# Optimization experiments

Hardware: AMD Instinct MI355X
Metric: run time of the kernel (lower is better)

## Reference

```python
import jax, jax.numpy as jnp
import numpy as np

HIDDEN = 4096
N_HEADS = 32
N_KV_HEADS = 8
HEAD_DIM = HIDDEN // N_HEADS  # 128
INTER = 11008
EPS = 1e-6
ROPE_THETA = 10000.0
B, S = 2, 2048


def setup_inputs() -> dict:
    key = jax.random.key(0)
    ks = jax.random.split(key, 8)
    sc = 0.02
    return {
        "hidden_states": jax.random.normal(ks[0], (B, S, HIDDEN), dtype=jnp.float32),
        "positions": jnp.arange(S, dtype=jnp.int32),
        "w_qkv": jax.random.normal(ks[1], (HIDDEN, (N_HEADS + 2 * N_KV_HEADS) * HEAD_DIM), dtype=jnp.float32) * sc,
        "w_o": jax.random.normal(ks[2], (N_HEADS * HEAD_DIM, HIDDEN), dtype=jnp.float32) * sc,
        "w_gate_up": jax.random.normal(ks[3], (HIDDEN, 2 * INTER), dtype=jnp.float32) * sc,
        "w_down": jax.random.normal(ks[4], (INTER, HIDDEN), dtype=jnp.float32) * sc,
        "ln1_w": jnp.ones((HIDDEN,), dtype=jnp.float32),
        "ln2_w": jnp.ones((HIDDEN,), dtype=jnp.float32),
    }


def _rms_norm(x, w):
    var = jnp.mean(jnp.square(x), axis=-1, keepdims=True)
    return x * jax.lax.rsqrt(var + EPS) * w


def _rope(x, positions):
    # x: [B, S, H, D]; NeoX-style rotary over full head_dim
    d = x.shape[-1]
    inv_freq = 1.0 / (ROPE_THETA ** (jnp.arange(0, d, 2, dtype=jnp.float32) / d))
    freqs = positions.astype(jnp.float32)[:, None] * inv_freq[None, :]  # [S, D/2]
    cos = jnp.cos(freqs)[None, :, None, :]
    sin = jnp.sin(freqs)[None, :, None, :]
    x1, x2 = jnp.split(x, 2, axis=-1)
    return jnp.concatenate([x1 * cos - x2 * sin, x2 * cos + x1 * sin], axis=-1)


def _decoder_layer(hidden_states, positions, w_qkv, w_o, w_gate_up, w_down, ln1_w, ln2_w):
    b, s, _ = hidden_states.shape
    scale = HEAD_DIM ** -0.5

    # --- attention block ---
    residual = hidden_states
    x = _rms_norm(hidden_states, ln1_w)
    qkv = x @ w_qkv
    q, k, v = jnp.split(qkv, [N_HEADS * HEAD_DIM, (N_HEADS + N_KV_HEADS) * HEAD_DIM], axis=-1)
    q = q.reshape(b, s, N_HEADS, HEAD_DIM)
    k = k.reshape(b, s, N_KV_HEADS, HEAD_DIM)
    v = v.reshape(b, s, N_KV_HEADS, HEAD_DIM)
    q = _rope(q, positions)
    k = _rope(k, positions)
    # GQA: expand kv heads
    g = N_HEADS // N_KV_HEADS
    k = jnp.repeat(k, g, axis=2)  # [B, S, H, D]
    v = jnp.repeat(v, g, axis=2)
    scores = jnp.einsum("bqhd,bkhd->bhqk", q, k) * scale
    causal = jnp.tril(jnp.ones((s, s), dtype=bool))
    scores = jnp.where(causal[None, None], scores, jnp.finfo(scores.dtype).min)
    probs = jax.nn.softmax(scores, axis=-1)
    attn = jnp.einsum("bhqk,bkhd->bqhd", probs, v).reshape(b, s, N_HEADS * HEAD_DIM)
    hidden_states = residual + attn @ w_o

    # --- MLP block (SwiGLU) ---
    residual = hidden_states
    x = _rms_norm(hidden_states, ln2_w)
    gate_up = x @ w_gate_up
    gate, up = jnp.split(gate_up, 2, axis=-1)
    hidden_states = residual + (jax.nn.silu(gate) * up) @ w_down
    return hidden_states


def reference(hidden_states, positions, w_qkv, w_o, w_gate_up, w_down, ln1_w, ln2_w):
    return _decoder_layer(hidden_states, positions, w_qkv, w_o, w_gate_up, w_down, ln1_w, ln2_w)
```

## Files before the change

### kernel.cpp

```cpp
#include <hip/hip_runtime.h>


typedef __attribute__((ext_vector_type(8))) short bf16x8;
typedef __attribute__((ext_vector_type(4))) float f32x4;

__device__ __forceinline__ ushort f2bf(float f) {
  unsigned u = __float_as_uint(f);
  return (ushort)((u + 0x7fffu + ((u >> 16) & 1u)) >> 16);
}
__device__ __forceinline__ float bf2f(ushort u) {
  union { unsigned u32; float f; } x; x.u32 = ((unsigned)u) << 16; return x.f;
}
__device__ __forceinline__ void gload16(const void* g, void* l) {
  __builtin_amdgcn_global_load_lds((__attribute__((address_space(1))) void*)g,
                                   (__attribute__((address_space(3))) void*)l,
                                   16, 0, 0);
}

#define BARRIER() asm volatile("s_barrier" ::: "memory")
#define WAIT_LGKM0() asm volatile("s_waitcnt lgkmcnt(0)" ::: "memory")
#define WAIT_VM8() asm volatile("s_waitcnt vmcnt(8)" ::: "memory")
#define WAIT_VM4() asm volatile("s_waitcnt vmcnt(4)" ::: "memory")
#define WAIT_VM0() asm volatile("s_waitcnt vmcnt(0)" ::: "memory")

__global__ __launch_bounds__(256) void rmsnorm_kernel(
    const float* __restrict__ x, const float* __restrict__ g,
    ushort* __restrict__ out) {
  const int row = blockIdx.x, t = threadIdx.x;
  const float4* xp = (const float4*)(x + (size_t)row * 4096);
  float4 v[4]; float ss = 0.f;
#pragma unroll
  for (int i = 0; i < 4; ++i) {
    v[i] = xp[t + i * 256];
    ss += v[i].x * v[i].x + v[i].y * v[i].y + v[i].z * v[i].z + v[i].w * v[i].w;
  }
#pragma unroll
  for (int m = 32; m; m >>= 1) ss += __shfl_xor(ss, m);
  __shared__ float red[4];
  if ((t & 63) == 0) red[t >> 6] = ss;
  __syncthreads();
  float inv = rsqrtf((red[0] + red[1] + red[2] + red[3]) * (1.f / 4096.f) + 1e-6f);
  const float4* gp = (const float4*)g;
  ushort* op = out + (size_t)row * 4096;
#pragma unroll
  for (int i = 0; i < 4; ++i) {
    float4 gv = gp[t + i * 256];
    ushort4 o;
    o.x = f2bf(v[i].x * inv * gv.x); o.y = f2bf(v[i].y * inv * gv.y);
    o.z = f2bf(v[i].z * inv * gv.z); o.w = f2bf(v[i].w * inv * gv.w);
    *(ushort4*)(op + (size_t)(t + i * 256) * 4) = o;
  }
}

__global__ __launch_bounds__(256) void transpose_cast_kernel(
    const float* __restrict__ in, ushort* __restrict__ out,
    int ld_in, int col_off, int R) {
  __shared__ ushort tile[64][68];
  const int t = threadIdx.x;
  const int r0 = blockIdx.x * 64, c0 = blockIdx.y * 64;
  const int rl = t >> 2, cl = (t & 3) * 16;
  const float* ip = in + (size_t)(r0 + rl) * ld_in + col_off + c0 + cl;
#pragma unroll
  for (int i = 0; i < 4; ++i) {
    float4 f = ((const float4*)ip)[i];
    tile[rl][cl + i * 4 + 0] = f2bf(f.x);
    tile[rl][cl + i * 4 + 1] = f2bf(f.y);
    tile[rl][cl + i * 4 + 2] = f2bf(f.z);
    tile[rl][cl + i * 4 + 3] = f2bf(f.w);
  }
  __syncthreads();
  union { ushort us[8]; uint4 v; } pk0, pk1;
#pragma unroll
  for (int j = 0; j < 8; ++j) pk0.us[j] = tile[cl + j][rl];
#pragma unroll
  for (int j = 0; j < 8; ++j) pk1.us[j] = tile[cl + 8 + j][rl];
  uint4* op = (uint4*)(out + (size_t)(c0 + rl) * R + r0 + cl);
  op[0] = pk0.v; op[1] = pk1.v;
}

template <typename OutT, bool RES>
__global__ __launch_bounds__(512, 2) void gemm256_kernel(
    const ushort* __restrict__ A, const ushort* __restrict__ Bt,
    OutT* __restrict__ C, const float* __restrict__ res,
    int M, int N, int K) {
  extern __shared__ ushort lds[];
  ushort* Al = lds;
  ushort* Bl = lds + 32768;
  const int t = threadIdx.x, l = t & 63, w = t >> 6;
  const int wr = w >> 2, wc = w & 3;
  const int lr = l & 15, lg = l >> 4;
  const int rhi = lr >> 3, rlo = lr & 7;
  const int srow = l >> 3, sg = (l & 7) ^ srow;

  const int nbx = N >> 8;
  const int nwg = nbx * (M >> 8);
  const int cpx = nwg >> 3;
  const int bid = (int)blockIdx.x;
  const int swz = (bid & 7) * cpx + (bid >> 3);
  const int n0 = (swz % nbx) << 8, m0 = (swz / nbx) << 8;

  const int lof0 = rhi * 512 + rlo * 64 + ((0 + lg) ^ rlo) * 8;
  const int lof1 = rhi * 512 + rlo * 64 + ((4 + lg) ^ rlo) * 8;

  const f32x4 fz = {0.f, 0.f, 0.f, 0.f};
  f32x4 acc[8][4];
#pragma unroll
  for (int i = 0; i < 8; ++i)
#pragma unroll
    for (int j = 0; j < 4; ++j) acc[i][j] = fz;
  bf16x8 a[8][2];
  bf16x8 bq[2][2];

  const ushort* Asrc = A + (size_t)(m0 + w * 8 + srow) * K + sg * 8;
  const ushort* Bsrc = Bt + (size_t)(n0 + w * 8 + srow) * K + sg * 8;
  const size_t rK64 = (size_t)64 * K, rK128 = (size_t)128 * K;
  ushort* Adst = Al + w * 512;
  ushort* Bdst = Bl + w * 512;

#define STAGE_A(buf, half, tile) do {                                   \
    const ushort* s_ = Asrc + (size_t)(half) * rK128 + ((tile) << 6);   \
    ushort* d_ = Adst + (buf) * 16384 + (half) * 8192;                  \
    gload16(s_, d_);                                                    \
    gload16(s_ + rK64, d_ + 4096);                                      \
  } while (0)
#define STAGE_B(buf, half, tile) do {                                   \
    const ushort* s_ = Bsrc + (size_t)(half) * rK128 + ((tile) << 6);   \
    ushort* d_ = Bdst + (buf) * 16384 + (half) * 8192;                  \
    gload16(s_, d_);                                                    \
    gload16(s_ + rK64, d_ + 4096);                                      \
  } while (0)
#define LDA4(AH, QM) do {                                                   \
    _Pragma("unroll") for (int mi_ = 0; mi_ < 4; ++mi_) {                   \
      a[(QM) * 4 + mi_][0] =                                                \
          *(const bf16x8*)((AH) + ((QM) * 4 + mi_) * 1024 + lof0);          \
      a[(QM) * 4 + mi_][1] =                                                \
          *(const bf16x8*)((AH) + ((QM) * 4 + mi_) * 1024 + lof1);          \
    } } while (0)
#define LDB2(BH, NQ) do {                                                   \
    _Pragma("unroll") for (int nj_ = 0; nj_ < 2; ++nj_) {                   \
      bq[nj_][0] = *(const bf16x8*)((BH) + ((NQ) * 2 + nj_) * 1024 + lof0); \
      bq[nj_][1] = *(const bf16x8*)((BH) + ((NQ) * 2 + nj_) * 1024 + lof1); \
    } } while (0)
#define MFMA16(QM, QN)                                                      \
    __builtin_amdgcn_s_setprio(1);                                          \
    _Pragma("unroll") for (int mi_ = 0; mi_ < 4; ++mi_)                     \
    _Pragma("unroll") for (int nj_ = 0; nj_ < 2; ++nj_) {                   \
      acc[(QM) * 4 + mi_][(QN) * 2 + nj_] =                                 \
          __builtin_amdgcn_mfma_f32_16x16x32_bf16(                          \
              a[(QM) * 4 + mi_][0], bq[nj_][0],                             \
              acc[(QM) * 4 + mi_][(QN) * 2 + nj_], 0, 0, 0);                \
      acc[(QM) * 4 + mi_][(QN) * 2 + nj_] =                                 \
          __builtin_amdgcn_mfma_f32_16x16x32_bf16(                          \
              a[(QM) * 4 + mi_][1], bq[nj_][1],                             \
              acc[(QM) * 4 + mi_][(QN) * 2 + nj_], 0, 0, 0);                \
    }                                                                       \
    __builtin_amdgcn_s_setprio(0);

  const ushort* A0h = Al + wr * 8192;
  const ushort* A1h = A0h + 16384;
  const ushort* B0h = Bl + (wc >> 1) * 8192 + (wc & 1) * 4096;
  const ushort* B1h = B0h + 16384;

  const int ntiles = K >> 6, nIter = K >> 7;
  STAGE_A(0, 0, 0); STAGE_A(0, 1, 0); STAGE_B(0, 0, 0); STAGE_B(0, 1, 0);
  STAGE_A(1, 0, 1); STAGE_A(1, 1, 1);
  WAIT_VM4(); BARRIER();

  for (int it = 0; it < nIter; ++it) {
    const int u = it * 2;
    LDA4(A0h, 0); LDB2(B0h, 0);
    STAGE_B(1, 0, u + 1);
    BARRIER(); WAIT_LGKM0(); MFMA16(0, 0); BARRIER();
    LDA4(A0h, 1);
    STAGE_B(1, 1, u + 1);
    BARRIER(); WAIT_LGKM0(); MFMA16(1, 0); BARRIER();
    LDB2(B0h, 1);
    if (u + 2 < ntiles) STAGE_A(0, 0, u + 2);
    BARRIER(); WAIT_LGKM0(); MFMA16(0, 1); BARRIER();
    if (u + 2 < ntiles) STAGE_A(0, 1, u + 2);
    BARRIER(); MFMA16(1, 1);
    if (u + 2 < ntiles) { WAIT_VM4(); } else { WAIT_VM0(); }
    BARRIER();
    LDA4(A1h, 0); LDB2(B1h, 0);
    if (u + 2 < ntiles) STAGE_B(0, 0, u + 2);
    BARRIER(); WAIT_LGKM0(); MFMA16(0, 0); BARRIER();
    LDA4(A1h, 1);
    if (u + 2 < ntiles) STAGE_B(0, 1, u + 2);
    BARRIER(); WAIT_LGKM0(); MFMA16(1, 0); BARRIER();
    LDB2(B1h, 1);
    if (u + 3 < ntiles) STAGE_A(1, 0, u + 3);
    BARRIER(); WAIT_LGKM0(); MFMA16(0, 1); BARRIER();
    if (u + 3 < ntiles) STAGE_A(1, 1, u + 3);
    BARRIER(); MFMA16(1, 1);
    WAIT_VM4(); BARRIER();
  }

#pragma unroll
  for (int mi = 0; mi < 8; ++mi)
#pragma unroll
    for (int ni = 0; ni < 4; ++ni)
#pragma unroll
      for (int r = 0; r < 4; ++r) {
        int row = m0 + wr * 128 + mi * 16 + lg * 4 + r;
        int col = n0 + wc * 64 + ni * 16 + lr;
        size_t idx = (size_t)row * N + col;
        float v = acc[mi][ni][r];
        if (RES) v += res[idx];
        if constexpr (sizeof(OutT) == 2) C[idx] = f2bf(v);
        else                             C[idx] = v;
      }
#undef STAGE_A
#undef STAGE_B
#undef LDA4
#undef LDB2
#undef MFMA16
}

__global__ void rope_table_kernel(const int* __restrict__ pos,
                                  float2* __restrict__ tab) {
  int idx = blockIdx.x * 256 + threadIdx.x;
  int s = idx >> 6, fi = idx & 63;
  float inv = (float)exp(-(double)(2 * fi) / 128.0 * 9.210340371976184);
  float a = (float)pos[s] * inv;
  tab[idx] = make_float2(cosf(a), sinf(a));
}

__global__ __launch_bounds__(256) void rope_scatter_kernel(
    const ushort* __restrict__ qkv, const float2* __restrict__ tab,
    ushort* __restrict__ Qr, ushort* __restrict__ Kr, ushort* __restrict__ Vt) {
  __shared__ ushort vt[64][132];
  const int t = threadIdx.x, tt = blockIdx.x, h = blockIdx.y;
  const int row = t >> 2, c = (t & 3) * 16;
  const int tok = tt * 64 + row;
  const int b = tok >> 11, s = tok & 2047;
  const ushort* ip = qkv + (size_t)tok * 6144 + h * 128;
  union U { uint4 v; ushort us[8]; };
  U a0, a1, b0, b1;
  a0.v = *(const uint4*)(ip + c);      a1.v = *(const uint4*)(ip + c + 8);
  b0.v = *(const uint4*)(ip + c + 64); b1.v = *(const uint4*)(ip + c + 72);
  if (h < 40) {
    U o0, o1, o2, o3;
#pragma unroll
    for (int j = 0; j < 8; ++j) {
      float2 cs = tab[s * 64 + c + j];
      float x1 = bf2f(a0.us[j]), x2 = bf2f(b0.us[j]);
      o0.us[j] = f2bf(x1 * cs.x - x2 * cs.y);
      o2.us[j] = f2bf(x2 * cs.x + x1 * cs.y);
    }
#pragma unroll
    for (int j = 0; j < 8; ++j) {
      float2 cs = tab[s * 64 + c + 8 + j];
      float x1 = bf2f(a1.us[j]), x2 = bf2f(b1.us[j]);
      o1.us[j] = f2bf(x1 * cs.x - x2 * cs.y);
      o3.us[j] = f2bf(x2 * cs.x + x1 * cs.y);
    }
    ushort* base;
    if (h < 32) base = Qr + ((size_t)((b * 32 + h) * 2048 + s)) * 128;
    else        base = Kr + ((size_t)((b * 8 + (h - 32)) * 2048 + s)) * 128;
    *(uint4*)(base + c)      = o0.v; *(uint4*)(base + c + 8)  = o1.v;
    *(uint4*)(base + c + 64) = o2.v; *(uint4*)(base + c + 72) = o3.v;
  } else {
    const int hv = h - 40;
#pragma unroll
    for (int j = 0; j < 8; ++j) {
      vt[row][c + j]      = a0.us[j]; vt[row][c + 8 + j]  = a1.us[j];
      vt[row][c + 64 + j] = b0.us[j]; vt[row][c + 72 + j] = b1.us[j];
    }
    __syncthreads();
    const int d = t >> 1, s0 = (t & 1) * 32, sb = (tt & 31) * 64;
    U w0, w1, w2, w3;
#pragma unroll
    for (int j = 0; j < 8; ++j) {
      w0.us[j] = vt[s0 + j][d];      w1.us[j] = vt[s0 + 8 + j][d];
      w2.us[j] = vt[s0 + 16 + j][d]; w3.us[j] = vt[s0 + 24 + j][d];
    }
    ushort* vb = Vt + ((size_t)((b * 8 + hv) * 128 + d)) * 2048 + sb + s0;
    *(uint4*)(vb) = w0.v;      *(uint4*)(vb + 8) = w1.v;
    *(uint4*)(vb + 16) = w2.v; *(uint4*)(vb + 24) = w3.v;
  }
}

__global__ __launch_bounds__(256) void attn_kernel(
    const ushort* __restrict__ Q, const ushort* __restrict__ K,
    const ushort* __restrict__ V, ushort* __restrict__ O) {
  extern __shared__ ushort sm[];
  ushort* Kl = sm;
  ushort* Vl = sm + 16384;
  ushort* Pl = sm + 32768;
  const int t = threadIdx.x, l = t & 63, w = t >> 6;
  const int lr = l & 15, lg = l >> 4;
  const int qt = blockIdx.x, h = blockIdx.y, b = blockIdx.z;
  const int hkv = h >> 2;
  const f32x4 fzero = {0.f, 0.f, 0.f, 0.f};

  const int rm = lr & 7;
  int ksw[4], vsw[2];
#pragma unroll
  for (int ks = 0; ks < 4; ++ks) ksw[ks] = ((ks * 4 + lg) ^ rm) * 8;
  vsw[0] = (lg ^ rm) * 8;
  vsw[1] = ((4 + lg) ^ rm) * 8;
  const int kcol = ((t & 15) ^ ((t >> 4) & 7)) * 8;
  const int vcol = ((t & 7) ^ ((t >> 3) & 7)) * 8;

  const ushort* qp =
      Q + ((size_t)((b * 32 + h) * 2048 + qt * 64 + w * 16 + lr)) * 128 + lg * 8;
  bf16x8 qf[4];
#pragma unroll
  for (int ks = 0; ks < 4; ++ks) qf[ks] = *(const bf16x8*)(qp + ks * 32);
  WAIT_VM0();

  const ushort* kg = K + ((size_t)(b * 8 + hkv)) * 2048 * 128;
  const ushort* vg = V + ((size_t)(b * 8 + hkv)) * 128 * 2048;

#define STAGE_KV(buf, s0_) do {                                              \
    _Pragma("unroll") for (int i_ = 0; i_ < 4; ++i_)                         \
      gload16(kg + (size_t)((s0_) + i_ * 16 + (t >> 4)) * 128 + kcol,        \
              (char*)Kl + (buf) * 16384 + i_ * 4096 + t * 16);               \
    _Pragma("unroll") for (int i_ = 0; i_ < 4; ++i_)                         \
      gload16(vg + (size_t)(i_ * 32 + (t >> 3)) * 2048 + (s0_) + vcol,       \
              (char*)Vl + (buf) * 16384 + i_ * 4096 + t * 16);               \
  } while (0)

  f32x4 accO[8];
#pragma unroll
  for (int i = 0; i < 8; ++i) accO[i] = fzero;
  float m_r[4] = {-1e30f, -1e30f, -1e30f, -1e30f};
  float l_r[4] = {0.f, 0.f, 0.f, 0.f};
  const float scale = 0.08838834764831845f;
  const int qrow = qt * 64 + w * 16 + lg * 4;

  STAGE_KV(0, 0);
  for (int j = 0; j <= qt; ++j) {
    if (j < qt) { STAGE_KV((j + 1) & 1, (j + 1) * 64); WAIT_VM8(); }
    else        { WAIT_VM0(); }
    BARRIER();
    const ushort* Kb = Kl + (j & 1) * 8192;
    const ushort* Vb = Vl + (j & 1) * 8192;

    f32x4 sc[4];
#pragma unroll
    for (int ni = 0; ni < 4; ++ni) sc[ni] = fzero;
    __builtin_amdgcn_s_setprio(1);
#pragma unroll
    for (int ni = 0; ni < 4; ++ni)
#pragma unroll
      for (int ks = 0; ks < 4; ++ks) {
        bf16x8 kf = *(const bf16x8*)(Kb + (ni * 16 + lr) * 128 + ksw[ks]);
        sc[ni] = __builtin_amdgcn_mfma_f32_16x16x32_bf16(qf[ks], kf, sc[ni], 0, 0, 0);
      }
    __builtin_amdgcn_s_setprio(0);
    if (j == qt) {
#pragma unroll
      for (int ni = 0; ni < 4; ++ni)
#pragma unroll
        for (int r = 0; r < 4; ++r) {
          float v = sc[ni][r] * scale;
          if (j * 64 + ni * 16 + lr > qrow + r) v = -1e30f;
          sc[ni][r] = v;
        }
    } else {
#pragma unroll
      for (int ni = 0; ni < 4; ++ni)
#pragma unroll
        for (int r = 0; r < 4; ++r) sc[ni][r] *= scale;
    }
    float mnew[4], fsc[4], lad[4];
#pragma unroll
    for (int r = 0; r < 4; ++r) {
      float mx = fmaxf(fmaxf(sc[0][r], sc[1][r]), fmaxf(sc[2][r], sc[3][r]));
#pragma unroll
      for (int m = 8; m; m >>= 1) mx = fmaxf(mx, __shfl_xor(mx, m));
      mnew[r] = fmaxf(m_r[r], mx);
      fsc[r] = __expf(m_r[r] - mnew[r]);
      lad[r] = 0.f;
    }
#pragma unroll
    for (int ni = 0; ni < 4; ++ni)
#pragma unroll
      for (int r = 0; r < 4; ++r) {
        float p = __expf(sc[ni][r] - mnew[r]);
        sc[ni][r] = p;
        lad[r] += p;
      }
#pragma unroll
    for (int r = 0; r < 4; ++r) {
#pragma unroll
      for (int m = 8; m; m >>= 1) lad[r] += __shfl_xor(lad[r], m);
      l_r[r] = l_r[r] * fsc[r] + lad[r];
      m_r[r] = mnew[r];
    }
#pragma unroll
    for (int i = 0; i < 8; ++i)
#pragma unroll
      for (int r = 0; r < 4; ++r) accO[i][r] *= fsc[r];
#pragma unroll
    for (int ni = 0; ni < 4; ++ni)
#pragma unroll
      for (int r = 0; r < 4; ++r) {
        int prow = w * 16 + lg * 4 + r;
        int slot = (ni * 2 + (lr >> 3)) ^ (prow & 7);
        Pl[prow * 64 + slot * 8 + rm] = f2bf(sc[ni][r]);
      }
    WAIT_LGKM0();
    __builtin_amdgcn_s_setprio(1);
#pragma unroll
    for (int ks = 0; ks < 2; ++ks) {
      bf16x8 pf = *(const bf16x8*)(Pl + (w * 16 + lr) * 64 + vsw[ks]);
#pragma unroll
      for (int nf = 0; nf < 8; ++nf) {
        bf16x8 vf = *(const bf16x8*)(Vb + (nf * 16 + lr) * 64 + vsw[ks]);
        accO[nf] = __builtin_amdgcn_mfma_f32_16x16x32_bf16(pf, vf, accO[nf], 0, 0, 0);
      }
    }
    __builtin_amdgcn_s_setprio(0);
    BARRIER();
  }
#undef STAGE_KV
#pragma unroll
  for (int nf = 0; nf < 8; ++nf)
#pragma unroll
    for (int r = 0; r < 4; ++r) {
      int q = qt * 64 + w * 16 + lg * 4 + r;
      int d = nf * 16 + lr;
      float v = accO[nf][r] / l_r[r];
      O[((size_t)(b * 2048 + q)) * 4096 + h * 128 + d] = f2bf(v);
    }
}

__global__ void swiglu_kernel(ushort* __restrict__ gate,
                              const ushort* __restrict__ up, int n8) {
  union U { uint4 v; ushort us[8]; };
  for (int i = blockIdx.x * blockDim.x + threadIdx.x; i < n8;
       i += gridDim.x * blockDim.x) {
    U gv, uv, ov;
    gv.v = ((const uint4*)gate)[i];
    uv.v = ((const uint4*)up)[i];
#pragma unroll
    for (int j = 0; j < 8; ++j) {
      float x = bf2f(gv.us[j]);
      float y = bf2f(uv.us[j]);
      ov.us[j] = f2bf(x / (1.f + __expf(-x)) * y);
    }
    ((uint4*)gate)[i] = ov.v;
  }
}

#define OFF_W    ((size_t)0)
#define OFF_H1   ((size_t)90177536)
#define OFF_XN   ((size_t)157286400)
#define OFF_QKV  ((size_t)190840832)
#define OFF_TAB  ((size_t)241172480)
#define OFF_QR   ((size_t)242221056)
#define OFF_KR   ((size_t)275775488)
#define OFF_VT   ((size_t)284164096)
#define OFF_ATTN ((size_t)292552704)
#define OFF_GATE OFF_QKV
#define OFF_UP   ((size_t)326107136)
#define WS_NEED  ((size_t)416284672)

extern "C" void kernel_launch(void* const* d_in, const int* in_sizes, int n_in,
                              void* d_out, int out_size, void* d_ws,
                              size_t ws_size, hipStream_t stream) {
  (void)in_sizes; (void)n_in; (void)out_size;
  if (ws_size < WS_NEED) return;
  const float* hs     = (const float*)d_in[0];
  const int*   pos    = (const int*)d_in[1];
  const float* w_qkv  = (const float*)d_in[2];
  const float* w_o    = (const float*)d_in[3];
  const float* w_gu   = (const float*)d_in[4];
  const float* w_down = (const float*)d_in[5];
  const float* ln1    = (const float*)d_in[6];
  const float* ln2    = (const float*)d_in[7];
  float* out = (float*)d_out;
  char* ws = (char*)d_ws;

  ushort* W    = (ushort*)(ws + OFF_W);
  float*  h1   = (float*)(ws + OFF_H1);
  ushort* xn   = (ushort*)(ws + OFF_XN);
  ushort* qkv  = (ushort*)(ws + OFF_QKV);
  float2* tab  = (float2*)(ws + OFF_TAB);
  ushort* Qr   = (ushort*)(ws + OFF_QR);
  ushort* Kr   = (ushort*)(ws + OFF_KR);
  ushort* Vt   = (ushort*)(ws + OFF_VT);
  ushort* attn = (ushort*)(ws + OFF_ATTN);
  ushort* gate = (ushort*)(ws + OFF_GATE);
  ushort* up   = (ushort*)(ws + OFF_UP);

  auto kb = gemm256_kernel<ushort, false>;
  auto kf = gemm256_kernel<float, true>;
  hipFuncSetAttribute((const void*)kb, hipFuncAttributeMaxDynamicSharedMemorySize, 131072);
  hipFuncSetAttribute((const void*)kf, hipFuncAttributeMaxDynamicSharedMemorySize, 131072);
  hipFuncSetAttribute((const void*)attn_kernel, hipFuncAttributeMaxDynamicSharedMemorySize, 73728);

  rmsnorm_kernel<<<4096, 256, 0, stream>>>(hs, ln1, xn);
  transpose_cast_kernel<<<dim3(64, 96), 256, 0, stream>>>(w_qkv, W, 6144, 0, 4096);
  gemm256_kernel<ushort, false><<<384, 512, 131072, stream>>>(
      xn, W, qkv, nullptr, 4096, 6144, 4096);
  rope_table_kernel<<<512, 256, 0, stream>>>(pos, tab);
  rope_scatter_kernel<<<dim3(64, 48), 256, 0, stream>>>(qkv, tab, Qr, Kr, Vt);
  attn_kernel<<<dim3(32, 32, 2), 256, 73728, stream>>>(Qr, Kr, Vt, attn);
  transpose_cast_kernel<<<dim3(64, 64), 256, 0, stream>>>(w_o, W, 4096, 0, 4096);
  gemm256_kernel<float, true><<<256, 512, 131072, stream>>>(
      attn, W, h1, hs, 4096, 4096, 4096);

  rmsnorm_kernel<<<4096, 256, 0, stream>>>(h1, ln2, xn);
  transpose_cast_kernel<<<dim3(64, 172), 256, 0, stream>>>(w_gu, W, 22016, 0, 4096);
  gemm256_kernel<ushort, false><<<688, 512, 131072, stream>>>(
      xn, W, gate, nullptr, 4096, 11008, 4096);
  transpose_cast_kernel<<<dim3(64, 172), 256, 0, stream>>>(w_gu, W, 22016, 11008, 4096);
  gemm256_kernel<ushort, false><<<688, 512, 131072, stream>>>(
      xn, W, up, nullptr, 4096, 11008, 4096);
  swiglu_kernel<<<2048, 256, 0, stream>>>(gate, up, (4096 * 11008) / 8);
  transpose_cast_kernel<<<dim3(172, 64), 256, 0, stream>>>(w_down, W, 4096, 0, 11008);
  gemm256_kernel<float, true><<<256, 512, 131072, stream>>>(
      gate, W, out, h1, 4096, 4096, 11008);
}
```

Measured before the change: 1.911 ms.

## Fuse SwiGLU into up GEMM epilogue and streamline attention softmax

The separate SwiGLU kernel is removed and its work moves into the up-projection GEMM epilogue, which reads the bf16 gate tensor and writes the activated product. Attention now folds the softmax scale and log2e into Q, uses exp2, skips the rescale when the running max grows by at most 8, and computes row sums with an extra MFMA against a ones vector instead of shuffle reductions. The transpose tile padding also changes from 68 to 65. The cost is slightly lower precision from pre-scaling Q in bf16 and from the lazy rescale, and the 65-wide tile may cause misaligned or bank-conflicting LDS accesses.

```diff
diff --git a/kernel.cpp b/kernel.cpp
--- a/kernel.cpp
+++ b/kernel.cpp
@@ -55,7 +55,7 @@
 __global__ __launch_bounds__(256) void transpose_cast_kernel(
     const float* __restrict__ in, ushort* __restrict__ out,
     int ld_in, int col_off, int R) {
-  __shared__ ushort tile[64][68];
+  __shared__ ushort tile[64][65];
   const int t = threadIdx.x;
   const int r0 = blockIdx.x * 64, c0 = blockIdx.y * 64;
   const int rl = t >> 2, cl = (t & 3) * 16;
@@ -78,10 +78,10 @@
   op[0] = pk0.v; op[1] = pk1.v;
 }
 
-template <typename OutT, bool RES>
+template <int EPI>
 __global__ __launch_bounds__(512, 2) void gemm256_kernel(
     const ushort* __restrict__ A, const ushort* __restrict__ Bt,
-    OutT* __restrict__ C, const float* __restrict__ res,
+    void* __restrict__ Cv, const void* __restrict__ aux,
     int M, int N, int K) {
   extern __shared__ ushort lds[];
   ushort* Al = lds;
@@ -205,9 +205,15 @@
         int col = n0 + wc * 64 + ni * 16 + lr;
         size_t idx = (size_t)row * N + col;
         float v = acc[mi][ni][r];
-        if (RES) v += res[idx];
-        if constexpr (sizeof(OutT) == 2) C[idx] = f2bf(v);
-        else                             C[idx] = v;
+        if constexpr (EPI == 0) {
+          ((ushort*)Cv)[idx] = f2bf(v);
+        } else if constexpr (EPI == 1) {
+          ((float*)Cv)[idx] = v + ((const float*)aux)[idx];
+        } else {
+          float g = bf2f(((const ushort*)aux)[idx]);
+          float s = g / (1.f + __expf(-g));
+          ((ushort*)Cv)[idx] = f2bf(s * v);
+        }
       }
 #undef STAGE_A
 #undef STAGE_B
@@ -302,11 +308,20 @@
   const int kcol = ((t & 15) ^ ((t >> 4) & 7)) * 8;
   const int vcol = ((t & 7) ^ ((t >> 3) & 7)) * 8;
 
+  const float qscale = 0.08838834764831845f * 1.4426950408889634f;
   const ushort* qp =
       Q + ((size_t)((b * 32 + h) * 2048 + qt * 64 + w * 16 + lr)) * 128 + lg * 8;
   bf16x8 qf[4];
 #pragma unroll
-  for (int ks = 0; ks < 4; ++ks) qf[ks] = *(const bf16x8*)(qp + ks * 32);
+  for (int ks = 0; ks < 4; ++ks) {
+    bf16x8 raw = *(const bf16x8*)(qp + ks * 32);
+#pragma unroll
+    for (int j = 0; j < 8; ++j)
+      qf[ks][j] = (short)f2bf(bf2f((ushort)raw[j]) * qscale);
+  }
+  bf16x8 ones;
+#pragma unroll
+  for (int j = 0; j < 8; ++j) ones[j] = (short)0x3F80;
   WAIT_VM0();
 
   const ushort* kg = K + ((size_t)(b * 8 + hkv)) * 2048 * 128;
@@ -326,7 +341,6 @@
   for (int i = 0; i < 8; ++i) accO[i] = fzero;
   float m_r[4] = {-1e30f, -1e30f, -1e30f, -1e30f};
   float l_r[4] = {0.f, 0.f, 0.f, 0.f};
-  const float scale = 0.08838834764831845f;
   const int qrow = qt * 64 + w * 16 + lg * 4;
 
   STAGE_KV(0, 0);
@@ -353,55 +367,40 @@
 #pragma unroll
       for (int ni = 0; ni < 4; ++ni)
 #pragma unroll
-        for (int r = 0; r < 4; ++r) {
-          float v = sc[ni][r] * scale;
-          if (j * 64 + ni * 16 + lr > qrow + r) v = -1e30f;
-          sc[ni][r] = v;
-        }
-    } else {
-#pragma unroll
-      for (int ni = 0; ni < 4; ++ni)
-#pragma unroll
-        for (int r = 0; r < 4; ++r) sc[ni][r] *= scale;
-    }
-    float mnew[4], fsc[4], lad[4];
+        for (int r = 0; r < 4; ++r)
+          if (j * 64 + ni * 16 + lr > qrow + r) sc[ni][r] = -1e30f;
+    }
+    float mx[4];
 #pragma unroll
     for (int r = 0; r < 4; ++r) {
-      float mx = fmaxf(fmaxf(sc[0][r], sc[1][r]), fmaxf(sc[2][r], sc[3][r]));
-#pragma unroll
-      for (int m = 8; m; m >>= 1) mx = fmaxf(mx, __shfl_xor(mx, m));
-      mnew[r] = fmaxf(m_r[r], mx);
-      fsc[r] = __expf(m_r[r] - mnew[r]);
-      lad[r] = 0.f;
-    }
-#pragma unroll
-    for (int ni = 0; ni < 4; ++ni)
+      float v = fmaxf(fmaxf(sc[0][r], sc[1][r]), fmaxf(sc[2][r], sc[3][r]));
+#pragma unroll
+      for (int m = 8; m; m >>= 1) v = fmaxf(v, __shfl_xor(v, m));
+      mx[r] = v;
+    }
+    bool ok = mx[0] <= m_r[0] + 8.f && mx[1] <= m_r[1] + 8.f &&
+              mx[2] <= m_r[2] + 8.f && mx[3] <= m_r[3] + 8.f;
+    if (!__all(ok)) {
 #pragma unroll
       for (int r = 0; r < 4; ++r) {
-        float p = __expf(sc[ni][r] - mnew[r]);
-        sc[ni][r] = p;
-        lad[r] += p;
+        float mnew = fmaxf(m_r[r], mx[r]);
+        float fsc = exp2f(m_r[r] - mnew);
+        l_r[r] *= fsc;
+        m_r[r] = mnew;
+#pragma unroll
+        for (int i = 0; i < 8; ++i) accO[i][r] *= fsc;
       }
-#pragma unroll
-    for (int r = 0; r < 4; ++r) {
-#pragma unroll
-      for (int m = 8; m; m >>= 1) lad[r] += __shfl_xor(lad[r], m);
-      l_r[r] = l_r[r] * fsc[r] + lad[r];
-      m_r[r] = mnew[r];
-    }
-#pragma unroll
-    for (int i = 0; i < 8; ++i)
-#pragma unroll
-      for (int r = 0; r < 4; ++r) accO[i][r] *= fsc[r];
+    }
 #pragma unroll
     for (int ni = 0; ni < 4; ++ni)
 #pragma unroll
       for (int r = 0; r < 4; ++r) {
         int prow = w * 16 + lg * 4 + r;
         int slot = (ni * 2 + (lr >> 3)) ^ (prow & 7);
-        Pl[prow * 64 + slot * 8 + rm] = f2bf(sc[ni][r]);
+        Pl[prow * 64 + slot * 8 + rm] = f2bf(exp2f(sc[ni][r] - m_r[r]));
       }
     WAIT_LGKM0();
+    f32x4 accL = fzero;
     __builtin_amdgcn_s_setprio(1);
 #pragma unroll
     for (int ks = 0; ks < 2; ++ks) {
@@ -411,8 +410,11 @@
         bf16x8 vf = *(const bf16x8*)(Vb + (nf * 16 + lr) * 64 + vsw[ks]);
         accO[nf] = __builtin_amdgcn_mfma_f32_16x16x32_bf16(pf, vf, accO[nf], 0, 0, 0);
       }
+      accL = __builtin_amdgcn_mfma_f32_16x16x32_bf16(pf, ones, accL, 0, 0, 0);
     }
     __builtin_amdgcn_s_setprio(0);
+#pragma unroll
+    for (int r = 0; r < 4; ++r) l_r[r] += accL[r];
     BARRIER();
   }
 #undef STAGE_KV
@@ -425,24 +427,6 @@
       float v = accO[nf][r] / l_r[r];
       O[((size_t)(b * 2048 + q)) * 4096 + h * 128 + d] = f2bf(v);
     }
-}
-
-__global__ void swiglu_kernel(ushort* __restrict__ gate,
-                              const ushort* __restrict__ up, int n8) {
-  union U { uint4 v; ushort us[8]; };
-  for (int i = blockIdx.x * blockDim.x + threadIdx.x; i < n8;
-       i += gridDim.x * blockDim.x) {
-    U gv, uv, ov;
-    gv.v = ((const uint4*)gate)[i];
-    uv.v = ((const uint4*)up)[i];
-#pragma unroll
-    for (int j = 0; j < 8; ++j) {
-      float x = bf2f(gv.us[j]);
-      float y = bf2f(uv.us[j]);
-      ov.us[j] = f2bf(x / (1.f + __expf(-x)) * y);
-    }
-    ((uint4*)gate)[i] = ov.v;
-  }
 }
 
 #define OFF_W    ((size_t)0)
@@ -484,34 +468,27 @@
   ushort* Vt   = (ushort*)(ws + OFF_VT);
   ushort* attn = (ushort*)(ws + OFF_ATTN);
   ushort* gate = (ushort*)(ws + OFF_GATE);
-  ushort* up   = (ushort*)(ws + OFF_UP);
-
-  auto kb = gemm256_kernel<ushort, false>;
-  auto kf = gemm256_kernel<float, true>;
-  hipFuncSetAttribute((const void*)kb, hipFuncAttributeMaxDynamicSharedMemorySize, 131072);
-  hipFuncSetAttribute((const void*)kf, hipFuncAttributeMaxDynamicSharedMemorySize, 131072);
+  ushort* act  = (ushort*)(ws + OFF_UP);
+
+  hipFuncSetAttribute((const void*)gemm256_kernel<0>, hipFuncAttributeMaxDynamicSharedMemorySize, 131072);
+  hipFuncSetAttribute((const void*)gemm256_kernel<1>, hipFuncAttributeMaxDynamicSharedMemorySize, 131072);
+  hipFuncSetAttribute((const void*)gemm256_kernel<2>, hipFuncAttributeMaxDynamicSharedMemorySize, 131072);
   hipFuncSetAttribute((const void*)attn_kernel, hipFuncAttributeMaxDynamicSharedMemorySize, 73728);
 
   rmsnorm_kernel<<<4096, 256, 0, stream>>>(hs, ln1, xn);
   transpose_cast_kernel<<<dim3(64, 96), 256, 0, stream>>>(w_qkv, W, 6144, 0, 4096);
-  gemm256_kernel<ushort, false><<<384, 512, 131072, stream>>>(
-      xn, W, qkv, nullptr, 4096, 6144, 4096);
+  gemm256_kernel<0><<<384, 512, 131072, stream>>>(xn, W, qkv, nullptr, 4096, 6144, 4096);
   rope_table_kernel<<<512, 256, 0, stream>>>(pos, tab);
   rope_scatter_kernel<<<dim3(64, 48), 256, 0, stream>>>(qkv, tab, Qr, Kr, Vt);
   attn_kernel<<<dim3(32, 32, 2), 256, 73728, stream>>>(Qr, Kr, Vt, attn);
   transpose_cast_kernel<<<dim3(64, 64), 256, 0, stream>>>(w_o, W, 4096, 0, 4096);
-  gemm256_kernel<float, true><<<256, 512, 131072, stream>>>(
-      attn, W, h1, hs, 4096, 4096, 4096);
+  gemm256_kernel<1><<<256, 512, 131072, stream>>>(attn, W, h1, hs, 4096, 4096, 4096);
 
   rmsnorm_kernel<<<4096, 256, 0, stream>>>(h1, ln2, xn);
   transpose_cast_kernel<<<dim3(64, 172), 256, 0, stream>>>(w_gu, W, 22016, 0, 4096);
-  gemm256_kernel<ushort, false><<<688, 512, 131072, stream>>>(
-      xn, W, gate, nullptr, 4096, 11008, 4096);
+  gemm256_kernel<0><<<688, 512, 131072, stream>>>(xn, W, gate, nullptr, 4096, 11008, 4096);
   transpose_cast_kernel<<<dim3(64, 172), 256, 0, stream>>>(w_gu, W, 22016, 11008, 4096);
-  gemm256_kernel<ushort, false><<<688, 512, 131072, stream>>>(
-      xn, W, up, nullptr, 4096, 11008, 4096);
-  swiglu_kernel<<<2048, 256, 0, stream>>>(gate, up, (4096 * 11008) / 8);
+  gemm256_kernel<2><<<688, 512, 131072, stream>>>(xn, W, act, gate, 4096, 11008, 4096);
   transpose_cast_kernel<<<dim3(172, 64), 256, 0, stream>>>(w_down, W, 4096, 0, 11008);
-  gemm256_kernel<float, true><<<256, 512, 131072, stream>>>(
-      gate, W, out, h1, 4096, 4096, 11008);
-}
+  gemm256_kernel<1><<<256, 512, 131072, stream>>>(act, W, out, h1, 4096, 4096, 11008);
+}
```

New measurement: 1.883 ms. Within noise of the previous version (-1.4%).
